# Performance work log

Measured on AMD Instinct MI355X. Metric: run time of the kernel, lower is better.

The kernel has to match this reference:

```python
import jax, jax.numpy as jnp
import numpy as np


def setup_inputs() -> dict:
    key = jax.random.key(0)
    k1, k2, k3, k4, k5 = jax.random.split(key, 5)
    N_ALL, N, E, F, H, C = 100000, 50000, 300000, 256, 256, 3
    x_all = jax.random.normal(k1, (N_ALL, F), dtype=jnp.float32)
    n_id = jax.random.randint(k2, (N,), 0, N_ALL, dtype=jnp.int32)
    edge_index = jax.random.randint(k3, (2, E), 0, N, dtype=jnp.int32)
    # xavier_uniform for [in, out] = [256, 256]
    lim_s = float(np.sqrt(6.0 / (F + H)))
    W_sage = jax.random.uniform(k4, (F, H), dtype=jnp.float32, minval=-lim_s, maxval=lim_s)
    b_sage = jnp.zeros((H,), dtype=jnp.float32)
    lim_c = float(np.sqrt(6.0 / (H + C)))
    W_cls = jax.random.uniform(k5, (C, H), dtype=jnp.float32, minval=-lim_c, maxval=lim_c)
    b_cls = jnp.zeros((C,), dtype=jnp.float32)
    return {"x_all": x_all, "n_id": n_id, "edge_index": edge_index,
            "W_sage": W_sage, "b_sage": b_sage, "W_cls": W_cls, "b_cls": b_cls}


def reference(x_all, n_id, edge_index, W_sage, b_sage, W_cls, b_cls):
    # Gather sampled node features: x[data.n_id]
    x = x_all[n_id]                                   # [N, F]
    N = x.shape[0]
    src, dst = edge_index[0], edge_index[1]
    # SAGEConv (old PyG, aggr='mean', self-loops added): mean over {neighbors, self}
    msg = x[src]                                      # [E, F] gather
    agg = jax.ops.segment_sum(msg, dst, num_segments=N) + x          # sum incl. self-loop
    cnt = jax.ops.segment_sum(jnp.ones_like(dst, dtype=x.dtype), dst,
                              num_segments=N) + jnp.asarray(1.0, x.dtype)
    h = (agg / cnt[:, None]) @ W_sage + b_sage        # [N, 256]
    scores = h @ W_cls.T + b_cls                      # [N, 3]
    return jax.nn.log_softmax(scores, axis=1)
```

## Files before the change

### kernel.cpp

```cpp
#include <hip/hip_runtime.h>
#include <hip/hip_bf16.h>

#define F 256
#define CAP 64

__device__ __forceinline__ float bfbits2f(unsigned short u) {
    return __uint_as_float(((unsigned)u) << 16);
}
__device__ __forceinline__ float loadw(const void* __restrict__ w, int idx, int fp32m) {
    return fp32m ? ((const float*)w)[idx] : bfbits2f(((const unsigned short*)w)[idx]);
}
__device__ __forceinline__ int probe_fp32(const void* __restrict__ x_all) {
    unsigned short u = ((const unsigned short*)x_all)[(threadIdx.x & 63) * 2];
    float v = bfbits2f(u);
    unsigned long long m = __ballot(!(fabsf(v) < 100.0f));
    return (m != 0ULL) ? 1 : 0;
}

__global__ void setup_kernel(const void* __restrict__ x_all,
                             const void* __restrict__ W_sage, const void* __restrict__ b_sage,
                             const void* __restrict__ W_cls, const void* __restrict__ b_cls,
                             int* __restrict__ cnt, float* __restrict__ w0f,
                             float* __restrict__ w1f, float* __restrict__ w2f,
                             float* __restrict__ bc2, int* __restrict__ flag, int N) {
    int b = blockIdx.x;
    int t = threadIdx.x;
    int nz = (N + 255) / 256;
    if (b < nz) {
        int i = b * 256 + t;
        if (i < N) cnt[i] = 0;
        return;
    }
    if (b == nz) {
        if (t < 64) {
            int f = probe_fp32(x_all);
            if (t == 0) *flag = f;
        }
        return;
    }
    __shared__ int sflag;
    if (t < 64) {
        int f = probe_fp32(x_all);
        if (t == 0) sflag = f;
    }
    __syncthreads();
    int fp32m = sflag;

    if (b == nz + 1) {
        __shared__ float wc[3][F];
        #pragma unroll
        for (int c = 0; c < 3; ++c) wc[c][t] = loadw(W_cls, c * F + t, fp32m);
        __syncthreads();
        float s0 = 0.f, s1 = 0.f, s2 = 0.f;
        for (int j = 0; j < F; ++j) {
            float ws = loadw(W_sage, t * F + j, fp32m);
            s0 = fmaf(ws, wc[0][j], s0);
            s1 = fmaf(ws, wc[1][j], s1);
            s2 = fmaf(ws, wc[2][j], s2);
        }
        w0f[t] = s0; w1f[t] = s1; w2f[t] = s2;
    } else {
        __shared__ float r[4][3];
        int lane = t & 63, w = t >> 6;
        float bs = loadw(b_sage, t, fp32m);
        float p0 = bs * loadw(W_cls, 0 * F + t, fp32m);
        float p1 = bs * loadw(W_cls, 1 * F + t, fp32m);
        float p2 = bs * loadw(W_cls, 2 * F + t, fp32m);
        #pragma unroll
        for (int off = 32; off > 0; off >>= 1) {
            p0 += __shfl_xor(p0, off);
            p1 += __shfl_xor(p1, off);
            p2 += __shfl_xor(p2, off);
        }
        if (lane == 0) { r[w][0] = p0; r[w][1] = p1; r[w][2] = p2; }
        __syncthreads();
        if (t < 3) bc2[t] = r[0][t] + r[1][t] + r[2][t] + r[3][t] + loadw(b_cls, t, fp32m);
    }
}

__global__ __launch_bounds__(256) void stream_fill_kernel(
        const void* __restrict__ x_all, const int* __restrict__ n_id,
        const int* __restrict__ src, const int* __restrict__ dst,
        const float* __restrict__ w0f, const float* __restrict__ w1f,
        const float* __restrict__ w2f,
        float4* __restrict__ tall, int* __restrict__ cnt, int* __restrict__ bkt,
        const int* __restrict__ flag, int R, int E, int nTall) {
    int b = blockIdx.x;
    int t = threadIdx.x;
    if (b < nTall) {
        int fp32m = *flag;
        __shared__ __align__(16) float sw0[F], sw1[F], sw2[F];
        sw0[t] = w0f[t]; sw1[t] = w1f[t]; sw2[t] = w2f[t];
        __syncthreads();
        const float4* sw04 = (const float4*)sw0;
        const float4* sw14 = (const float4*)sw1;
        const float4* sw24 = (const float4*)sw2;

        int row = b * 256 + t;
        if (row >= R) return;
        float a0 = 0.f, a1 = 0.f, a2 = 0.f;
        if (fp32m) {
            const float4* xr = (const float4*)((const float*)x_all + (size_t)row * F);
            #pragma unroll 8
            for (int j = 0; j < 64; ++j) {
                float4 v = xr[j];
                float4 u0 = sw04[j], u1 = sw14[j], u2 = sw24[j];
                a0 += v.x * u0.x + v.y * u0.y + v.z * u0.z + v.w * u0.w;
                a1 += v.x * u1.x + v.y * u1.y + v.z * u1.z + v.w * u1.w;
                a2 += v.x * u2.x + v.y * u2.y + v.z * u2.z + v.w * u2.w;
            }
        } else {
            const uint4* xr = (const uint4*)((const unsigned short*)x_all + (size_t)row * F);
            #pragma unroll 4
            for (int j = 0; j < 32; ++j) {
                uint4 q = xr[j];
                float4 u0a = sw04[2 * j], u0b = sw04[2 * j + 1];
                float4 u1a = sw14[2 * j], u1b = sw14[2 * j + 1];
                float4 u2a = sw24[2 * j], u2b = sw24[2 * j + 1];
                float v0 = bfbits2f((unsigned short)(q.x & 0xffff));
                float v1 = bfbits2f((unsigned short)(q.x >> 16));
                float v2 = bfbits2f((unsigned short)(q.y & 0xffff));
                float v3 = bfbits2f((unsigned short)(q.y >> 16));
                float v4 = bfbits2f((unsigned short)(q.z & 0xffff));
                float v5 = bfbits2f((unsigned short)(q.z >> 16));
                float v6 = bfbits2f((unsigned short)(q.w & 0xffff));
                float v7 = bfbits2f((unsigned short)(q.w >> 16));
                a0 += v0*u0a.x + v1*u0a.y + v2*u0a.z + v3*u0a.w
                    + v4*u0b.x + v5*u0b.y + v6*u0b.z + v7*u0b.w;
                a1 += v0*u1a.x + v1*u1a.y + v2*u1a.z + v3*u1a.w
                    + v4*u1b.x + v5*u1b.y + v6*u1b.z + v7*u1b.w;
                a2 += v0*u2a.x + v1*u2a.y + v2*u2a.z + v3*u2a.w
                    + v4*u2b.x + v5*u2b.y + v6*u2b.z + v7*u2b.w;
            }
        }
        tall[row] = make_float4(a0, a1, a2, 0.f);
    } else {
        int e = (b - nTall) * 256 + t;
        if (e < E) {
            int s = src[e];
            int d = dst[e];
            int rid = n_id[s];
            int p = atomicAdd(&cnt[d], 1);
            if (p < CAP) bkt[((size_t)d << 6) + p] = rid;
        }
    }
}

__global__ void final_kernel(const float4* __restrict__ tall, const int* __restrict__ n_id,
                             const int* __restrict__ cnt, const int* __restrict__ bkt,
                             const float* __restrict__ bc2, void* __restrict__ out,
                             const int* __restrict__ flag, int N) {
    int fp32m = *flag;
    int n = blockIdx.x * blockDim.x + threadIdx.x;
    if (n >= N) return;
    int dt = cnt[n];
    int d = dt < CAP ? dt : CAP;
    const int* bk = bkt + ((size_t)n << 6);
    float4 tv = tall[n_id[n]];
    float a0 = tv.x, a1 = tv.y, a2 = tv.z;
    for (int e = 0; e < d; e += 4) {
        int rem = d - e;
        int i0 = bk[e];
        int i1 = (rem > 1) ? bk[e + 1] : i0;
        int i2 = (rem > 2) ? bk[e + 2] : i0;
        int i3 = (rem > 3) ? bk[e + 3] : i0;
        float4 v0 = tall[i0];
        float4 v1 = tall[i1];
        float4 v2 = tall[i2];
        float4 v3 = tall[i3];
        a0 += v0.x; a1 += v0.y; a2 += v0.z;
        if (rem > 1) { a0 += v1.x; a1 += v1.y; a2 += v1.z; }
        if (rem > 2) { a0 += v2.x; a1 += v2.y; a2 += v2.z; }
        if (rem > 3) { a0 += v3.x; a1 += v3.y; a2 += v3.z; }
    }
    float inv = 1.0f / (float)(dt + 1);
    float s0 = a0 * inv + bc2[0];
    float s1 = a1 * inv + bc2[1];
    float s2 = a2 * inv + bc2[2];
    float mx = fmaxf(s0, fmaxf(s1, s2));
    float lse = mx + logf(expf(s0 - mx) + expf(s1 - mx) + expf(s2 - mx));
    if (fp32m) {
        float* o = (float*)out;
        o[(size_t)n * 3 + 0] = s0 - lse;
        o[(size_t)n * 3 + 1] = s1 - lse;
        o[(size_t)n * 3 + 2] = s2 - lse;
    } else {
        __hip_bfloat16* o = (__hip_bfloat16*)out;
        o[(size_t)n * 3 + 0] = __float2bfloat16(s0 - lse);
        o[(size_t)n * 3 + 1] = __float2bfloat16(s1 - lse);
        o[(size_t)n * 3 + 2] = __float2bfloat16(s2 - lse);
    }
}

extern "C" void kernel_launch(void* const* d_in, const int* in_sizes, int n_in,
                              void* d_out, int out_size, void* d_ws, size_t ws_size,
                              hipStream_t stream) {
    const void* x_all  = d_in[0];
    const int*  n_id   = (const int*)d_in[1];
    const int*  eidx   = (const int*)d_in[2];
    const void* W_sage = d_in[3];
    const void* b_sage = d_in[4];
    const void* W_cls  = d_in[5];
    const void* b_cls  = d_in[6];

    int R = in_sizes[0] / F;
    int N = in_sizes[1];
    int E = in_sizes[2] / 2;
    const int* src = eidx;
    const int* dst = eidx + E;

    float4* tall = (float4*)d_ws;
    int* cnt  = (int*)(tall + R);
    int* bkt  = cnt + N;
    float* w0f = (float*)(bkt + ((size_t)N << 6));
    float* w1f = w0f + F;
    float* w2f = w1f + F;
    float* bc2 = w2f + F;
    int* flag  = (int*)(bc2 + 4);

    int nz = (N + 255) / 256;
    setup_kernel<<<nz + 3, 256, 0, stream>>>(x_all, W_sage, b_sage, W_cls, b_cls,
                                             cnt, w0f, w1f, w2f, bc2, flag, N);
    int nTall = (R + 255) / 256;
    int nFill = (E + 255) / 256;
    stream_fill_kernel<<<nTall + nFill, 256, 0, stream>>>(
        x_all, n_id, src, dst, w0f, w1f, w2f, tall, cnt, bkt, flag, R, E, nTall);
    final_kernel<<<(N + 255) / 256, 256, 0, stream>>>(tall, n_id, cnt, bkt, bc2,
                                                      d_out, flag, N);
}
```

Before: 221.7 us.

## Project only sampled rows with 4 threads per row and vectorize bucket reads

The projection stage now covers only the N sampled nodes, gathered through n_id, instead of all R rows of x_all, which halves the feature bytes read. Each row is split across 4 threads reading interleaved 16-byte chunks, so accesses coalesce better, and the partial sums are combined with shuffles. Buckets now store local source indices, and the final kernel reads them as int4, which removes the n_id indirection there. The trade-off is a gathered, random-row read pattern and duplicate reads when n_id repeats rows.

New measurement: 204.2 us. 1.09x faster.

```diff
diff --git a/kernel.cpp b/kernel.cpp
--- a/kernel.cpp
+++ b/kernel.cpp
@@ -83,11 +83,11 @@
         const int* __restrict__ src, const int* __restrict__ dst,
         const float* __restrict__ w0f, const float* __restrict__ w1f,
         const float* __restrict__ w2f,
-        float4* __restrict__ tall, int* __restrict__ cnt, int* __restrict__ bkt,
-        const int* __restrict__ flag, int R, int E, int nTall) {
+        float4* __restrict__ hc, int* __restrict__ cnt, int* __restrict__ bkt,
+        const int* __restrict__ flag, int N, int E, int nH) {
     int b = blockIdx.x;
     int t = threadIdx.x;
-    if (b < nTall) {
+    if (b < nH) {
         int fp32m = *flag;
         __shared__ __align__(16) float sw0[F], sw1[F], sw2[F];
         sw0[t] = w0f[t]; sw1[t] = w1f[t]; sw2[t] = w2f[t];
@@ -96,27 +96,31 @@
         const float4* sw14 = (const float4*)sw1;
         const float4* sw24 = (const float4*)sw2;
 
-        int row = b * 256 + t;
-        if (row >= R) return;
+        int n = b * 64 + (t >> 2);
+        if (n >= N) return;
+        int k = t & 3;
+        int rid = n_id[n];
         float a0 = 0.f, a1 = 0.f, a2 = 0.f;
         if (fp32m) {
-            const float4* xr = (const float4*)((const float*)x_all + (size_t)row * F);
-            #pragma unroll 8
-            for (int j = 0; j < 64; ++j) {
-                float4 v = xr[j];
-                float4 u0 = sw04[j], u1 = sw14[j], u2 = sw24[j];
+            const float4* xr = (const float4*)((const float*)x_all + (size_t)rid * F);
+            #pragma unroll
+            for (int j = 0; j < 16; ++j) {
+                int c = j * 4 + k;
+                float4 v = xr[c];
+                float4 u0 = sw04[c], u1 = sw14[c], u2 = sw24[c];
                 a0 += v.x * u0.x + v.y * u0.y + v.z * u0.z + v.w * u0.w;
                 a1 += v.x * u1.x + v.y * u1.y + v.z * u1.z + v.w * u1.w;
                 a2 += v.x * u2.x + v.y * u2.y + v.z * u2.z + v.w * u2.w;
             }
         } else {
-            const uint4* xr = (const uint4*)((const unsigned short*)x_all + (size_t)row * F);
-            #pragma unroll 4
-            for (int j = 0; j < 32; ++j) {
-                uint4 q = xr[j];
-                float4 u0a = sw04[2 * j], u0b = sw04[2 * j + 1];
-                float4 u1a = sw14[2 * j], u1b = sw14[2 * j + 1];
-                float4 u2a = sw24[2 * j], u2b = sw24[2 * j + 1];
+            const uint4* xr = (const uint4*)((const unsigned short*)x_all + (size_t)rid * F);
+            #pragma unroll
+            for (int j = 0; j < 8; ++j) {
+                int c = j * 4 + k;
+                uint4 q = xr[c];
+                float4 u0a = sw04[2 * c], u0b = sw04[2 * c + 1];
+                float4 u1a = sw14[2 * c], u1b = sw14[2 * c + 1];
+                float4 u2a = sw24[2 * c], u2b = sw24[2 * c + 1];
                 float v0 = bfbits2f((unsigned short)(q.x & 0xffff));
                 float v1 = bfbits2f((unsigned short)(q.x >> 16));
                 float v2 = bfbits2f((unsigned short)(q.y & 0xffff));
@@ -133,20 +137,22 @@
                     + v4*u2b.x + v5*u2b.y + v6*u2b.z + v7*u2b.w;
             }
         }
-        tall[row] = make_float4(a0, a1, a2, 0.f);
+        a0 += __shfl_xor(a0, 1); a0 += __shfl_xor(a0, 2);
+        a1 += __shfl_xor(a1, 1); a1 += __shfl_xor(a1, 2);
+        a2 += __shfl_xor(a2, 1); a2 += __shfl_xor(a2, 2);
+        if (k == 0) hc[n] = make_float4(a0, a1, a2, 0.f);
     } else {
-        int e = (b - nTall) * 256 + t;
+        int e = (b - nH) * 256 + t;
         if (e < E) {
             int s = src[e];
             int d = dst[e];
-            int rid = n_id[s];
             int p = atomicAdd(&cnt[d], 1);
-            if (p < CAP) bkt[((size_t)d << 6) + p] = rid;
-        }
-    }
-}
-
-__global__ void final_kernel(const float4* __restrict__ tall, const int* __restrict__ n_id,
+            if (p < CAP) bkt[((size_t)d << 6) + p] = s;
+        }
+    }
+}
+
+__global__ void final_kernel(const float4* __restrict__ hc,
                              const int* __restrict__ cnt, const int* __restrict__ bkt,
                              const float* __restrict__ bc2, void* __restrict__ out,
                              const int* __restrict__ flag, int N) {
@@ -155,19 +161,20 @@
     if (n >= N) return;
     int dt = cnt[n];
     int d = dt < CAP ? dt : CAP;
-    const int* bk = bkt + ((size_t)n << 6);
-    float4 tv = tall[n_id[n]];
+    const int4* bk4 = (const int4*)(bkt + ((size_t)n << 6));
+    float4 tv = hc[n];
     float a0 = tv.x, a1 = tv.y, a2 = tv.z;
     for (int e = 0; e < d; e += 4) {
         int rem = d - e;
-        int i0 = bk[e];
-        int i1 = (rem > 1) ? bk[e + 1] : i0;
-        int i2 = (rem > 2) ? bk[e + 2] : i0;
-        int i3 = (rem > 3) ? bk[e + 3] : i0;
-        float4 v0 = tall[i0];
-        float4 v1 = tall[i1];
-        float4 v2 = tall[i2];
-        float4 v3 = tall[i3];
+        int4 q = bk4[e >> 2];
+        int i0 = q.x;
+        int i1 = (rem > 1) ? q.y : i0;
+        int i2 = (rem > 2) ? q.z : i0;
+        int i3 = (rem > 3) ? q.w : i0;
+        float4 v0 = hc[i0];
+        float4 v1 = hc[i1];
+        float4 v2 = hc[i2];
+        float4 v3 = hc[i3];
         a0 += v0.x; a1 += v0.y; a2 += v0.z;
         if (rem > 1) { a0 += v1.x; a1 += v1.y; a2 += v1.z; }
         if (rem > 2) { a0 += v2.x; a1 += v2.y; a2 += v2.z; }
@@ -203,14 +210,13 @@
     const void* W_cls  = d_in[5];
     const void* b_cls  = d_in[6];
 
-    int R = in_sizes[0] / F;
     int N = in_sizes[1];
     int E = in_sizes[2] / 2;
     const int* src = eidx;
     const int* dst = eidx + E;
 
-    float4* tall = (float4*)d_ws;
-    int* cnt  = (int*)(tall + R);
+    float4* hc = (float4*)d_ws;
+    int* cnt  = (int*)(hc + N);
     int* bkt  = cnt + N;
     float* w0f = (float*)(bkt + ((size_t)N << 6));
     float* w1f = w0f + F;
@@ -221,10 +227,10 @@
     int nz = (N + 255) / 256;
     setup_kernel<<<nz + 3, 256, 0, stream>>>(x_all, W_sage, b_sage, W_cls, b_cls,
                                              cnt, w0f, w1f, w2f, bc2, flag, N);
-    int nTall = (R + 255) / 256;
+    int nH = (N + 63) / 64;
     int nFill = (E + 255) / 256;
-    stream_fill_kernel<<<nTall + nFill, 256, 0, stream>>>(
-        x_all, n_id, src, dst, w0f, w1f, w2f, tall, cnt, bkt, flag, R, E, nTall);
-    final_kernel<<<(N + 255) / 256, 256, 0, stream>>>(tall, n_id, cnt, bkt, bc2,
+    stream_fill_kernel<<<nH + nFill, 256, 0, stream>>>(
+        x_all, n_id, src, dst, w0f, w1f, w2f, hc, cnt, bkt, flag, N, E, nH);
+    final_kernel<<<(N + 255) / 256, 256, 0, stream>>>(hc, cnt, bkt, bc2,
                                                       d_out, flag, N);
 }
```
